# Performance work log

Hardware: AMD Instinct MI355X
Metric: run time of the kernel (lower is better)

Reference implementation:

```python
import jax, jax.numpy as jnp
import numpy as np

B, S, F = 64, 512, 128   # batch, seq_len, raw feature dim
D = 512                  # dense_units
U = 1024                 # enc_units


def setup_inputs() -> dict:
    key = jax.random.key(0)
    k = jax.random.split(key, 6)
    x = jax.random.normal(k[0], (B, S, F), dtype=jnp.float32)
    dense_W = jax.random.normal(k[1], (F, D), dtype=jnp.float32) * (1.0 / np.sqrt(F))
    dense_b = jnp.zeros((D,), dtype=jnp.float32)
    Wx = jax.random.normal(k[2], (D, 4 * U), dtype=jnp.float32) * (1.0 / np.sqrt(D))
    Wh = jax.random.normal(k[3], (U, 4 * U), dtype=jnp.float32) * (1.0 / np.sqrt(U))
    b = jnp.zeros((4 * U,), dtype=jnp.float32)
    return {"x": x, "dense_W": dense_W, "dense_b": dense_b, "Wx": Wx, "Wh": Wh, "b": b}


def reference(x, dense_W, dense_b, Wx, Wh, b):
    # Dense projection (linear activation, as in Keras Dense default)
    h_in = jnp.einsum('bsf,fd->bsd', x, dense_W) + dense_b  # [B,S,D]

    # Precompute input contribution to all gates for every timestep
    gx = jnp.einsum('bsd,dg->bsg', h_in, Wx) + b            # [B,S,4U]
    gx_t = jnp.transpose(gx, (1, 0, 2))                     # [S,B,4U] for scan

    def step(carry, gxt):
        h_prev, c_prev = carry
        z = gxt + h_prev @ Wh                               # [B,4U]
        i, f, g, o = jnp.split(z, 4, axis=-1)               # Keras gate order i,f,g,o
        i = jax.nn.sigmoid(i)
        f = jax.nn.sigmoid(f)
        g = jnp.tanh(g)
        o = jax.nn.sigmoid(o)
        c = f * c_prev + i * g
        h = o * jnp.tanh(c)
        return (h, c), h

    h0 = jnp.zeros((x.shape[0], U), dtype=x.dtype)
    c0 = jnp.zeros((x.shape[0], U), dtype=x.dtype)
    (_, _), hs = jax.lax.scan(step, (h0, c0), gx_t)         # hs: [S,B,U]
    output = jnp.transpose(hs, (1, 0, 2))                   # [B,S,U], return_sequences=True
    return output
```

## Files before the change

kernel.cpp:

```cpp
#include <hip/hip_runtime.h>
#include <math.h>


#define BB 64
#define SS 512
#define FF 128
#define DD 512
#define UU 1024
#define GG 4096
#define CH 32

__device__ __forceinline__ float sigmoidf_(float v) {
    return 1.0f / (1.0f + __expf(-v));
}
__device__ __forceinline__ float tanhf_(float v) {
    float e = __expf(2.0f * v);
    return 1.0f - 2.0f / (e + 1.0f);
}

__global__ __launch_bounds__(256) void fuse_w(const float* __restrict__ dW,
                                              const float* __restrict__ Wx,
                                              float* __restrict__ Wf) {
    int tid = blockIdx.x * 256 + threadIdx.x;
    int g = tid & (GG - 1);
    int f = tid >> 12;
    const float* wr = dW + f * DD;
    float acc = 0.0f;
#pragma unroll 4
    for (int d = 0; d < DD; ++d)
        acc = fmaf(wr[d], Wx[(size_t)d * GG + g], acc);
    Wf[(size_t)f * GG + g] = acc;
}

__global__ __launch_bounds__(256) void fuse_b(const float* __restrict__ db,
                                              const float* __restrict__ Wx,
                                              const float* __restrict__ bias,
                                              float* __restrict__ bf) {
    int g = blockIdx.x * 256 + threadIdx.x;
    float acc = bias[g];
#pragma unroll 4
    for (int d = 0; d < DD; ++d)
        acc = fmaf(db[d], Wx[(size_t)d * GG + g], acc);
    bf[g] = acc;
}

__global__ __launch_bounds__(512) void gx_chunk(const float* __restrict__ x,
                                                const float* __restrict__ Wf,
                                                const float* __restrict__ bf,
                                                float* __restrict__ gxc, int s0) {
    __shared__ float xs[64 * 129];
    const int sl = blockIdx.x & (CH - 1);
    const int gt = blockIdx.x / CH;
    const int s  = s0 + sl;

    for (int i = threadIdx.x; i < 64 * 128; i += 512) {
        int bb = i >> 7, kk = i & 127;
        xs[bb * 129 + kk] = x[((size_t)bb * SS + s) * FF + kk];
    }
    __syncthreads();

    const int wid = threadIdx.x >> 6;
    const int b   = threadIdx.x & 63;
    const int g0  = __builtin_amdgcn_readfirstlane(gt * 256 + wid * 32);

    float acc[32];
#pragma unroll
    for (int i = 0; i < 32; ++i) acc[i] = bf[g0 + i];

    const float* wp = Wf + g0;
    const float* xp = xs + b * 129;
#pragma unroll 4
    for (int k = 0; k < FF; ++k) {
        float xv = xp[k];
#pragma unroll
        for (int i = 0; i < 32; i += 4) {
            float4 w = *(const float4*)(wp + i);
            acc[i + 0] = fmaf(w.x, xv, acc[i + 0]);
            acc[i + 1] = fmaf(w.y, xv, acc[i + 1]);
            acc[i + 2] = fmaf(w.z, xv, acc[i + 2]);
            acc[i + 3] = fmaf(w.w, xv, acc[i + 3]);
        }
        wp += GG;
    }
    float* op = gxc + ((size_t)sl * 64 + b) * GG + g0;
#pragma unroll
    for (int i = 0; i < 32; i += 4)
        *(float4*)(op + i) = make_float4(acc[i], acc[i + 1], acc[i + 2], acc[i + 3]);
}

__global__ __launch_bounds__(1024, 4) void lstm_step(const float* __restrict__ Wh,
                                                     const float* __restrict__ gxc,
                                                     float* __restrict__ out,
                                                     float* __restrict__ cbuf,
                                                     const float* __restrict__ hprev,
                                                     float* __restrict__ hnext,
                                                     int t, int tc) {
    __shared__ float zl[16 * 1024];
    __shared__ float zr[1024];
    const int utile = blockIdx.x & 63;
    const int btile = blockIdx.x >> 6;
    const int u0 = utile * 16;
    const int wid  = threadIdx.x >> 6;
    const int lane = threadIdx.x & 63;
    const int u_l  = lane & 15;
    const int bgrp = lane >> 4;

    float acc[4][4];
#pragma unroll
    for (int i = 0; i < 4; ++i)
#pragma unroll
        for (int g = 0; g < 4; ++g) acc[i][g] = 0.0f;

    if (t > 0) {
        const float* hp = hprev + (size_t)(wid * 64) * 64 + btile * 16 + bgrp * 4;
        const float* wp = Wh + (size_t)(wid * 64) * GG + u0 + u_l;
#pragma unroll 4
        for (int k = 0; k < 64; ++k) {
            const float4 h4 = *(const float4*)hp;
            float w0 = wp[0], w1 = wp[UU], w2 = wp[2 * UU], w3 = wp[3 * UU];
            float hv[4] = {h4.x, h4.y, h4.z, h4.w};
#pragma unroll
            for (int i = 0; i < 4; ++i) {
                acc[i][0] = fmaf(hv[i], w0, acc[i][0]);
                acc[i][1] = fmaf(hv[i], w1, acc[i][1]);
                acc[i][2] = fmaf(hv[i], w2, acc[i][2]);
                acc[i][3] = fmaf(hv[i], w3, acc[i][3]);
            }
            hp += 64;
            wp += GG;
        }
    }
#pragma unroll
    for (int g = 0; g < 4; ++g) {
        *(float4*)&zl[wid * 1024 + g * 256 + u_l * 16 + bgrp * 4] =
            make_float4(acc[0][g], acc[1][g], acc[2][g], acc[3][g]);
    }
    __syncthreads();

    {
        float v = 0.0f;
#pragma unroll
        for (int w = 0; w < 16; ++w) v += zl[w * 1024 + threadIdx.x];
        zr[threadIdx.x] = v;
    }
    __syncthreads();

    if (threadIdx.x < 256) {
        const int b_l  = threadIdx.x >> 4;
        const int u_l2 = threadIdx.x & 15;
        const int bb = btile * 16 + b_l;
        const int uu = u0 + u_l2;

        const float* gp = gxc + ((size_t)tc * 64 + bb) * GG + uu;
        float z[4];
#pragma unroll
        for (int g = 0; g < 4; ++g)
            z[g] = zr[g * 256 + u_l2 * 16 + b_l] + gp[g * UU];

        float iv = sigmoidf_(z[0]);
        float fv = sigmoidf_(z[1]);
        float gv = tanhf_(z[2]);
        float ov = sigmoidf_(z[3]);

        float* cp = cbuf + (size_t)uu * 64 + bb;
        float cv = fv * (*cp) + iv * gv;
        *cp = cv;
        float hv = ov * tanhf_(cv);

        out[((size_t)bb * SS + t) * UU + uu] = hv;
        hnext[(size_t)uu * 64 + bb] = hv;
    }
}

extern "C" void kernel_launch(void* const* d_in, const int* in_sizes, int n_in,
                              void* d_out, int out_size, void* d_ws, size_t ws_size,
                              hipStream_t stream) {
    const float* x    = (const float*)d_in[0];
    const float* dW   = (const float*)d_in[1];
    const float* db   = (const float*)d_in[2];
    const float* Wx   = (const float*)d_in[3];
    const float* Wh   = (const float*)d_in[4];
    const float* bias = (const float*)d_in[5];
    float* out = (float*)d_out;

    char* ws = (char*)d_ws;
    size_t off = 0;
    float* Wf   = (float*)(ws + off); off += (size_t)FF * GG * 4;
    float* bf   = (float*)(ws + off); off += (size_t)GG * 4;
    float* cbuf = (float*)(ws + off); off += (size_t)BB * UU * 4;
    float* hT0  = (float*)(ws + off); off += (size_t)BB * UU * 4;
    float* hT1  = (float*)(ws + off); off += (size_t)BB * UU * 4;
    float* gxc  = (float*)(ws + off);

    hipMemsetAsync(cbuf, 0, (size_t)BB * UU * 4, stream);
    fuse_w<<<(FF * GG) / 256, 256, 0, stream>>>(dW, Wx, Wf);
    fuse_b<<<GG / 256, 256, 0, stream>>>(db, Wx, bias, bf);

    float* bufs[2] = {hT0, hT1};
    for (int c = 0; c < SS / CH; ++c) {
        gx_chunk<<<16 * CH, 512, 0, stream>>>(x, Wf, bf, gxc, c * CH);
        for (int tt = 0; tt < CH; ++tt) {
            int t = c * CH + tt;
            lstm_step<<<256, 1024, 0, stream>>>(Wh, gxc, out, cbuf,
                                                bufs[(t + 1) & 1], bufs[t & 1], t, tt);
        }
    }
}
```

Baseline: 10.20 ms.

## Replace per-step launches with persistent cooperative LSTM kernel and grid barrier

Replaces the 512 per-timestep lstm_step launches and the chunked gx_chunk precompute with a single cooperative persistent kernel. It loops over time internally and synchronises the whole grid through an atomic barrier. The input projection (x·Wf) is folded into each step's GEMV, using a transposed x and gate-interleaved Wh/Wf layouts that allow float4 weight loads. The goal is to remove launch overhead and the gx round-trip through global memory. In exchange it adds a spin barrier per step and more FMA work on the step's critical path.

```diff
diff --git a/kernel.cpp b/kernel.cpp
--- a/kernel.cpp
+++ b/kernel.cpp
@@ -8,7 +8,7 @@
 #define DD 512
 #define UU 1024
 #define GG 4096
-#define CH 32
+#define NBLK 256
 
 __device__ __forceinline__ float sigmoidf_(float v) {
     return 1.0f / (1.0f + __expf(-v));
@@ -20,16 +20,16 @@
 
 __global__ __launch_bounds__(256) void fuse_w(const float* __restrict__ dW,
                                               const float* __restrict__ Wx,
-                                              float* __restrict__ Wf) {
+                                              float* __restrict__ Wf4) {
     int tid = blockIdx.x * 256 + threadIdx.x;
-    int g = tid & (GG - 1);
+    int gcol = tid & (GG - 1);
     int f = tid >> 12;
     const float* wr = dW + f * DD;
     float acc = 0.0f;
 #pragma unroll 4
     for (int d = 0; d < DD; ++d)
-        acc = fmaf(wr[d], Wx[(size_t)d * GG + g], acc);
-    Wf[(size_t)f * GG + g] = acc;
+        acc = fmaf(wr[d], Wx[(size_t)d * GG + gcol], acc);
+    Wf4[((size_t)f * UU + (gcol & (UU - 1))) * 4 + (gcol >> 10)] = acc;
 }
 
 __global__ __launch_bounds__(256) void fuse_b(const float* __restrict__ db,
@@ -44,59 +44,78 @@
     bf[g] = acc;
 }
 
-__global__ __launch_bounds__(512) void gx_chunk(const float* __restrict__ x,
-                                                const float* __restrict__ Wf,
-                                                const float* __restrict__ bf,
-                                                float* __restrict__ gxc, int s0) {
+__global__ __launch_bounds__(256) void repack_wh(const float* __restrict__ Wh,
+                                                 float* __restrict__ Wh4) {
+    size_t tid = (size_t)blockIdx.x * 256 + threadIdx.x;
+    int gcol = (int)(tid & (GG - 1));
+    int k = (int)(tid >> 12);
+    Wh4[((size_t)k * UU + (gcol & (UU - 1))) * 4 + (gcol >> 10)] = Wh[tid];
+}
+
+__global__ __launch_bounds__(256) void transpose_x(const float* __restrict__ x,
+                                                   float* __restrict__ xT) {
     __shared__ float xs[64 * 129];
-    const int sl = blockIdx.x & (CH - 1);
-    const int gt = blockIdx.x / CH;
-    const int s  = s0 + sl;
-
-    for (int i = threadIdx.x; i < 64 * 128; i += 512) {
-        int bb = i >> 7, kk = i & 127;
-        xs[bb * 129 + kk] = x[((size_t)bb * SS + s) * FF + kk];
+    const int s = blockIdx.x;
+    for (int i = threadIdx.x; i < 64 * 128; i += 256) {
+        int b = i >> 7, k = i & 127;
+        xs[b * 129 + k] = x[((size_t)b * SS + s) * FF + k];
     }
     __syncthreads();
-
-    const int wid = threadIdx.x >> 6;
-    const int b   = threadIdx.x & 63;
-    const int g0  = __builtin_amdgcn_readfirstlane(gt * 256 + wid * 32);
-
-    float acc[32];
-#pragma unroll
-    for (int i = 0; i < 32; ++i) acc[i] = bf[g0 + i];
-
-    const float* wp = Wf + g0;
-    const float* xp = xs + b * 129;
-#pragma unroll 4
-    for (int k = 0; k < FF; ++k) {
-        float xv = xp[k];
-#pragma unroll
-        for (int i = 0; i < 32; i += 4) {
-            float4 w = *(const float4*)(wp + i);
-            acc[i + 0] = fmaf(w.x, xv, acc[i + 0]);
-            acc[i + 1] = fmaf(w.y, xv, acc[i + 1]);
-            acc[i + 2] = fmaf(w.z, xv, acc[i + 2]);
-            acc[i + 3] = fmaf(w.w, xv, acc[i + 3]);
-        }
-        wp += GG;
-    }
-    float* op = gxc + ((size_t)sl * 64 + b) * GG + g0;
-#pragma unroll
-    for (int i = 0; i < 32; i += 4)
-        *(float4*)(op + i) = make_float4(acc[i], acc[i + 1], acc[i + 2], acc[i + 3]);
-}
-
-__global__ __launch_bounds__(1024, 4) void lstm_step(const float* __restrict__ Wh,
-                                                     const float* __restrict__ gxc,
-                                                     float* __restrict__ out,
-                                                     float* __restrict__ cbuf,
-                                                     const float* __restrict__ hprev,
-                                                     float* __restrict__ hnext,
-                                                     int t, int tc) {
-    __shared__ float zl[16 * 1024];
+    for (int i = threadIdx.x; i < 64 * 128; i += 256) {
+        int k = i >> 6, b = i & 63;
+        xT[((size_t)s * FF + k) * 64 + b] = xs[b * 129 + k];
+    }
+}
+
+__device__ __forceinline__ void fma16(float (&acc)[4][4], float4 h4, float4 w4) {
+    acc[0][0] = fmaf(h4.x, w4.x, acc[0][0]);
+    acc[0][1] = fmaf(h4.x, w4.y, acc[0][1]);
+    acc[0][2] = fmaf(h4.x, w4.z, acc[0][2]);
+    acc[0][3] = fmaf(h4.x, w4.w, acc[0][3]);
+    acc[1][0] = fmaf(h4.y, w4.x, acc[1][0]);
+    acc[1][1] = fmaf(h4.y, w4.y, acc[1][1]);
+    acc[1][2] = fmaf(h4.y, w4.z, acc[1][2]);
+    acc[1][3] = fmaf(h4.y, w4.w, acc[1][3]);
+    acc[2][0] = fmaf(h4.z, w4.x, acc[2][0]);
+    acc[2][1] = fmaf(h4.z, w4.y, acc[2][1]);
+    acc[2][2] = fmaf(h4.z, w4.z, acc[2][2]);
+    acc[2][3] = fmaf(h4.z, w4.w, acc[2][3]);
+    acc[3][0] = fmaf(h4.w, w4.x, acc[3][0]);
+    acc[3][1] = fmaf(h4.w, w4.y, acc[3][1]);
+    acc[3][2] = fmaf(h4.w, w4.z, acc[3][2]);
+    acc[3][3] = fmaf(h4.w, w4.w, acc[3][3]);
+}
+
+__device__ __forceinline__ void grid_barrier(unsigned* bar) {
+    __syncthreads();
+    if (threadIdx.x == 0) {
+        __threadfence();
+        unsigned g = __hip_atomic_load(&bar[1], __ATOMIC_SEQ_CST, __HIP_MEMORY_SCOPE_AGENT);
+        unsigned old = __hip_atomic_fetch_add(&bar[0], 1u, __ATOMIC_SEQ_CST, __HIP_MEMORY_SCOPE_AGENT);
+        if (old == NBLK - 1) {
+            __hip_atomic_store(&bar[0], 0u, __ATOMIC_RELAXED, __HIP_MEMORY_SCOPE_AGENT);
+            __hip_atomic_store(&bar[1], g + 1u, __ATOMIC_RELEASE, __HIP_MEMORY_SCOPE_AGENT);
+        } else {
+            while (__hip_atomic_load(&bar[1], __ATOMIC_RELAXED, __HIP_MEMORY_SCOPE_AGENT) == g)
+                __builtin_amdgcn_s_sleep(2);
+        }
+        __threadfence();
+    }
+    __syncthreads();
+}
+
+__global__ __launch_bounds__(1024, 4) void lstm_persist(
+    const float* __restrict__ xT,
+    const float* __restrict__ Wh4,
+    const float* __restrict__ Wf4,
+    const float* __restrict__ bfb,
+    float* __restrict__ out,
+    float* __restrict__ cbuf,
+    float* h0, float* h1,
+    unsigned* bar) {
+    __shared__ __align__(16) float zl[8 * 1024];
     __shared__ float zr[1024];
+
     const int utile = blockIdx.x & 63;
     const int btile = blockIdx.x >> 6;
     const int u0 = utile * 16;
@@ -104,71 +123,97 @@
     const int lane = threadIdx.x & 63;
     const int u_l  = lane & 15;
     const int bgrp = lane >> 4;
-
-    float acc[4][4];
-#pragma unroll
-    for (int i = 0; i < 4; ++i)
-#pragma unroll
-        for (int g = 0; g < 4; ++g) acc[i][g] = 0.0f;
-
-    if (t > 0) {
-        const float* hp = hprev + (size_t)(wid * 64) * 64 + btile * 16 + bgrp * 4;
-        const float* wp = Wh + (size_t)(wid * 64) * GG + u0 + u_l;
+    const int bbase = btile * 16 + bgrp * 4;
+
+    const float* wfx = Wf4 + ((size_t)(wid * 8) * UU + u0 + u_l) * 4;
+    const float* whb = Wh4 + ((size_t)(wid * 64) * UU + u0 + u_l) * 4;
+
+    for (int t = 0; t < SS; ++t) {
+        const float* hprev = (t & 1) ? h0 : h1;
+        float* hnext       = (t & 1) ? h1 : h0;
+
+        float acc[4][4];
+#pragma unroll
+        for (int i = 0; i < 4; ++i)
+#pragma unroll
+            for (int g = 0; g < 4; ++g) acc[i][g] = 0.0f;
+
+        {
+            const float* xp = xT + ((size_t)t * FF + wid * 8) * 64 + bbase;
+            const float* wp = wfx;
+#pragma unroll 2
+            for (int k = 0; k < 8; ++k) {
+                float4 h4 = *(const float4*)xp;
+                float4 w4 = *(const float4*)wp;
+                fma16(acc, h4, w4);
+                xp += 64;
+                wp += UU * 4;
+            }
+        }
+        if (t > 0) {
+            const float* hp = hprev + (size_t)(wid * 64) * 64 + bbase;
+            const float* wp = whb;
 #pragma unroll 4
-        for (int k = 0; k < 64; ++k) {
-            const float4 h4 = *(const float4*)hp;
-            float w0 = wp[0], w1 = wp[UU], w2 = wp[2 * UU], w3 = wp[3 * UU];
-            float hv[4] = {h4.x, h4.y, h4.z, h4.w};
-#pragma unroll
-            for (int i = 0; i < 4; ++i) {
-                acc[i][0] = fmaf(hv[i], w0, acc[i][0]);
-                acc[i][1] = fmaf(hv[i], w1, acc[i][1]);
-                acc[i][2] = fmaf(hv[i], w2, acc[i][2]);
-                acc[i][3] = fmaf(hv[i], w3, acc[i][3]);
+            for (int k = 0; k < 64; ++k) {
+                float4 h4 = *(const float4*)hp;
+                float4 w4 = *(const float4*)wp;
+                fma16(acc, h4, w4);
+                hp += 64;
+                wp += UU * 4;
             }
-            hp += 64;
-            wp += GG;
-        }
-    }
-#pragma unroll
-    for (int g = 0; g < 4; ++g) {
-        *(float4*)&zl[wid * 1024 + g * 256 + u_l * 16 + bgrp * 4] =
-            make_float4(acc[0][g], acc[1][g], acc[2][g], acc[3][g]);
-    }
-    __syncthreads();
-
-    {
-        float v = 0.0f;
-#pragma unroll
-        for (int w = 0; w < 16; ++w) v += zl[w * 1024 + threadIdx.x];
-        zr[threadIdx.x] = v;
-    }
-    __syncthreads();
-
-    if (threadIdx.x < 256) {
-        const int b_l  = threadIdx.x >> 4;
-        const int u_l2 = threadIdx.x & 15;
-        const int bb = btile * 16 + b_l;
-        const int uu = u0 + u_l2;
-
-        const float* gp = gxc + ((size_t)tc * 64 + bb) * GG + uu;
-        float z[4];
-#pragma unroll
-        for (int g = 0; g < 4; ++g)
-            z[g] = zr[g * 256 + u_l2 * 16 + b_l] + gp[g * UU];
-
-        float iv = sigmoidf_(z[0]);
-        float fv = sigmoidf_(z[1]);
-        float gv = tanhf_(z[2]);
-        float ov = sigmoidf_(z[3]);
-
-        float* cp = cbuf + (size_t)uu * 64 + bb;
-        float cv = fv * (*cp) + iv * gv;
-        *cp = cv;
-        float hv = ov * tanhf_(cv);
-
-        out[((size_t)bb * SS + t) * UU + uu] = hv;
-        hnext[(size_t)uu * 64 + bb] = hv;
+        }
+
+        if (wid < 8) {
+#pragma unroll
+            for (int g = 0; g < 4; ++g)
+                *(float4*)&zl[wid * 1024 + g * 256 + u_l * 16 + bgrp * 4] =
+                    make_float4(acc[0][g], acc[1][g], acc[2][g], acc[3][g]);
+        }
+        __syncthreads();
+        if (wid >= 8) {
+#pragma unroll
+            for (int g = 0; g < 4; ++g) {
+                float* p = &zl[(wid - 8) * 1024 + g * 256 + u_l * 16 + bgrp * 4];
+                float4 v = *(float4*)p;
+                v.x += acc[0][g]; v.y += acc[1][g]; v.z += acc[2][g]; v.w += acc[3][g];
+                *(float4*)p = v;
+            }
+        }
+        __syncthreads();
+        {
+            float v = 0.0f;
+#pragma unroll
+            for (int w = 0; w < 8; ++w) v += zl[w * 1024 + threadIdx.x];
+            zr[threadIdx.x] = v;
+        }
+        __syncthreads();
+
+        if (threadIdx.x < 256) {
+            const int bl = threadIdx.x >> 4;
+            const int ul = threadIdx.x & 15;
+            const int bb = btile * 16 + bl;
+            const int uu = u0 + ul;
+
+            float z0 = zr[0 * 256 + ul * 16 + bl] + bfb[uu];
+            float z1 = zr[1 * 256 + ul * 16 + bl] + bfb[uu + UU];
+            float z2 = zr[2 * 256 + ul * 16 + bl] + bfb[uu + 2 * UU];
+            float z3 = zr[3 * 256 + ul * 16 + bl] + bfb[uu + 3 * UU];
+
+            float iv = sigmoidf_(z0);
+            float fv = sigmoidf_(z1);
+            float gv = tanhf_(z2);
+            float ov = sigmoidf_(z3);
+
+            float* cp = cbuf + (size_t)uu * 64 + bb;
+            float cv = fv * (*cp) + iv * gv;
+            *cp = cv;
+            float hv = ov * tanhf_(cv);
+
+            out[((size_t)bb * SS + t) * UU + uu] = hv;
+            hnext[(size_t)uu * 64 + bb] = hv;
+        }
+
+        if (t != SS - 1) grid_barrier(bar);
     }
 }
 
@@ -185,24 +230,23 @@
 
     char* ws = (char*)d_ws;
     size_t off = 0;
-    float* Wf   = (float*)(ws + off); off += (size_t)FF * GG * 4;
-    float* bf   = (float*)(ws + off); off += (size_t)GG * 4;
+    float* Wh4 = (float*)(ws + off); off += (size_t)UU * UU * 4 * 4;
+    float* xT  = (float*)(ws + off); off += (size_t)SS * FF * 64 * 4;
+    float* Wf4 = (float*)(ws + off); off += (size_t)FF * UU * 4 * 4;
+    float* bf  = (float*)(ws + off); off += (size_t)GG * 4;
     float* cbuf = (float*)(ws + off); off += (size_t)BB * UU * 4;
-    float* hT0  = (float*)(ws + off); off += (size_t)BB * UU * 4;
-    float* hT1  = (float*)(ws + off); off += (size_t)BB * UU * 4;
-    float* gxc  = (float*)(ws + off);
+    float* h0  = (float*)(ws + off); off += (size_t)BB * UU * 4;
+    float* h1  = (float*)(ws + off); off += (size_t)BB * UU * 4;
+    unsigned* bar = (unsigned*)(ws + off);
 
     hipMemsetAsync(cbuf, 0, (size_t)BB * UU * 4, stream);
-    fuse_w<<<(FF * GG) / 256, 256, 0, stream>>>(dW, Wx, Wf);
+    hipMemsetAsync(bar, 0, 2 * sizeof(unsigned), stream);
+    fuse_w<<<(FF * GG) / 256, 256, 0, stream>>>(dW, Wx, Wf4);
     fuse_b<<<GG / 256, 256, 0, stream>>>(db, Wx, bias, bf);
-
-    float* bufs[2] = {hT0, hT1};
-    for (int c = 0; c < SS / CH; ++c) {
-        gx_chunk<<<16 * CH, 512, 0, stream>>>(x, Wf, bf, gxc, c * CH);
-        for (int tt = 0; tt < CH; ++tt) {
-            int t = c * CH + tt;
-            lstm_step<<<256, 1024, 0, stream>>>(Wh, gxc, out, cbuf,
-                                                bufs[(t + 1) & 1], bufs[t & 1], t, tt);
-        }
-    }
-}
+    repack_wh<<<(UU * GG) / 256, 256, 0, stream>>>(Wh, Wh4);
+    transpose_x<<<SS, 256, 0, stream>>>(x, xT);
+
+    void* args[] = {(void*)&xT, (void*)&Wh4, (void*)&Wf4, (void*)&bf, (void*)&out,
+                    (void*)&cbuf, (void*)&h0, (void*)&h1, (void*)&bar};
+    hipLaunchCooperativeKernel((void*)lstm_persist, dim3(NBLK), dim3(1024), args, 0, stream);
+}
```

New measurement: 26.09 ms. 156% more time.
